# Kernel tuning notes

Measured on AMD Instinct MI355X. Metric: run time of the kernel, lower is better.

Reference implementation:

```python
import jax, jax.numpy as jnp
import numpy as np

DIM = 1536
NH = 12
HD = DIM // NH  # 128
FF, HH, WW = 32, 8, 12
L = FF * HH * WW  # 3072
WIN = (8, 4, 4)  # block of 128 tokens
BLK = WIN[0] * WIN[1] * WIN[2]


def rms_norm(x, g, eps=1e-5):
    # matches RMSNorm: normalize in fp32, scale by weight
    v = jnp.mean(jnp.square(x), axis=-1, keepdims=True)
    return x * jax.lax.rsqrt(v + eps) * g


def rope(x, freqs, n):
    # x: [B,S,D]; freqs: [S,1,HD/2,2] (cos,sin); complex rotation on pairs
    B, S, D = x.shape
    xr = x.reshape(B, S, n, D // n // 2, 2)
    c, s = freqs[..., 0], freqs[..., 1]        # [S,1,HD/2] broadcast over B,n
    a, b = xr[..., 0], xr[..., 1]
    out = jnp.stack([a * c - b * s, a * s + b * c], axis=-1)
    return out.reshape(B, S, D)


def partition3d(x, f, h, w):
    # [B,f,h,w,D] -> [B, nblocks, 128, D], block order (f/8, h/4, w/4)
    B, D = x.shape[0], x.shape[-1]
    wf, wh, ww = WIN
    x = x.reshape(B, f // wf, wf, h // wh, wh, w // ww, ww, D)
    x = x.transpose(0, 1, 3, 5, 2, 4, 6, 7)
    return x.reshape(B, -1, BLK, D)


def reverse3d(xw, f, h, w):
    # [B, nblocks, 128, D] -> [B, f*h*w, D]
    B, D = xw.shape[0], xw.shape[-1]
    wf, wh, ww = WIN
    x = xw.reshape(B, f // wf, h // wh, w // ww, wf, wh, ww, D)
    x = x.transpose(0, 1, 4, 2, 5, 3, 6, 7)
    return x.reshape(B, f * h * w, D)


def block_mask(f, h, w):
    # build_local_block_mask_3d: spatial mask is all-ones; temporal = context|local
    seqlen = f // WIN[0]
    nb_sp = (h // WIN[1]) * (w // WIN[2])
    stride = WIN[0]
    ctx_idx = (6 + stride - 1) // stride - 1          # context_frames=6
    radius = (5 + stride - 1) // stride               # temp_window_frames=5
    t = jnp.arange(seqlen)
    mt = (t[None, :] <= ctx_idx) | (jnp.abs(t[:, None] - t[None, :]) <= radius)
    # expand temporal block mask over spatial blocks -> [nb, nb]
    return jnp.repeat(jnp.repeat(mt, nb_sp, axis=0), nb_sp, axis=1)


def setup_inputs() -> dict:
    key = jax.random.key(0)
    ks = jax.random.split(key, 8)
    x = jax.random.normal(ks[0], (1, L, DIM), jnp.float32)
    ang = jax.random.uniform(ks[1], (L, 1, HD // 2), jnp.float32, 0.0, 2.0 * np.pi)
    freqs = jnp.stack([jnp.cos(ang), jnp.sin(ang)], axis=-1)  # [L,1,64,2]
    sc = 1.0 / np.sqrt(DIM)
    Wq = jax.random.normal(ks[2], (DIM, DIM), jnp.float32) * sc
    Wk = jax.random.normal(ks[3], (DIM, DIM), jnp.float32) * sc
    Wv = jax.random.normal(ks[4], (DIM, DIM), jnp.float32) * sc
    Wo = jax.random.normal(ks[5], (DIM, DIM), jnp.float32) * sc
    zeros = jnp.zeros((DIM,), jnp.float32)
    ones = jnp.ones((DIM,), jnp.float32)
    return {"x": x, "freqs": freqs, "Wq": Wq, "bq": zeros, "Wk": Wk, "bk": zeros,
            "Wv": Wv, "bv": zeros, "Wo": Wo, "bo": zeros, "g_q": ones, "g_k": ones,
            "f": FF, "h": HH, "w": WW, "local_range": 18}


def reference(x, freqs, Wq, bq, Wk, bk, Wv, bv, Wo, bo, g_q, g_k, f, h, w, local_range):
    B, S, D = x.shape
    q = rms_norm(x @ Wq + bq, g_q, eps=1e-5)
    k = rms_norm(x @ Wk + bk, g_k, eps=1e-5)
    v = x @ Wv + bv
    q = rope(q, freqs, NH)
    k = rope(k, freqs, NH)
    # window partition and flatten back to a reordered sequence
    qs = partition3d(q.reshape(B, f, h, w, D), f, h, w).reshape(B, S, D)
    ks_ = partition3d(k.reshape(B, f, h, w, D), f, h, w).reshape(B, S, D)
    vs = partition3d(v.reshape(B, f, h, w, D), f, h, w).reshape(B, S, D)
    bm = block_mask(f, h, w)                       # [nb, nb] bool
    tok_mask = jnp.repeat(jnp.repeat(bm, BLK, 0), BLK, 1)  # [S, S]
    qh = qs.reshape(B, S, NH, HD).transpose(0, 2, 1, 3)
    kh = ks_.reshape(B, S, NH, HD).transpose(0, 2, 1, 3)
    vh = vs.reshape(B, S, NH, HD).transpose(0, 2, 1, 3)
    scores = jnp.einsum('bhqd,bhkd->bhqk', qh, kh) / np.sqrt(HD)
    scores = jnp.where(tok_mask[None, None], scores, -jnp.inf)
    attn = jax.nn.softmax(scores, axis=-1)
    out = jnp.einsum('bhqk,bhkd->bhqd', attn, vh)
    out = out.transpose(0, 2, 1, 3).reshape(B, S, D)
    out = reverse3d(out.reshape(B, -1, BLK, D), f, h, w)  # undo window reorder
    return out @ Wo + bo
```

## Files before the change

### kernel.cpp

```cpp
#include <hip/hip_runtime.h>
#include <hip/hip_bf16.h>
#include <math.h>

#define S_LEN 3072
#define DMODEL 1536
#define NQKV 4608
#define NHEAD 12
#define HDIM 128
#define NSPLIT 3

typedef __attribute__((ext_vector_type(8))) short bf16x8;
typedef __attribute__((ext_vector_type(4))) float f32x4;

__device__ __forceinline__ void gload_lds16(const void* g, void* lds) {
  __builtin_amdgcn_global_load_lds(
      (const __attribute__((address_space(1))) unsigned int*)g,
      (__attribute__((address_space(3))) unsigned int*)lds, 16, 0, 0);
}

__device__ __forceinline__ int invperm(int p) {
  int blk = p >> 7;
  int w   = p & 127;
  int fb  = blk / 6;
  int rem = blk - fb * 6;
  int hb  = rem / 3;
  int wb  = rem - hb * 3;
  int fi  = fb * 8 + (w >> 4);
  int hi  = hb * 4 + ((w >> 2) & 3);
  int wi  = wb * 4 + (w & 3);
  return (fi * 8 + hi) * 12 + wi;
}

__device__ __forceinline__ int fwdperm(int s) {
  int fi = s / 96;
  int rem = s - fi * 96;
  int hi = rem / 12;
  int wi = rem - hi * 12;
  int fb = fi >> 3, wf = fi & 7;
  int hb = hi >> 2, wh = hi & 3;
  int wb = wi >> 2, ww = wi & 3;
  return ((fb * 2 + hb) * 3 + wb) * 128 + wf * 16 + wh * 4 + ww;
}

__device__ __forceinline__ void store_out(float* p, float v) { *p = v; }
__device__ __forceinline__ void store_out(__hip_bfloat16* p, float v) { *p = __float2bfloat16(v); }

__global__ __launch_bounds__(256) void convert_bias(
    const float* __restrict__ in, __hip_bfloat16* __restrict__ out,
    const float* __restrict__ bq, const float* __restrict__ bk,
    const float* __restrict__ bv, float* __restrict__ bqkv)
{
  if (blockIdx.x < 4608) {
    int i = blockIdx.x * 256 + threadIdx.x;
    float4 v = ((const float4*)in)[i];
    __hip_bfloat16 b[4] = {__float2bfloat16(v.x), __float2bfloat16(v.y),
                           __float2bfloat16(v.z), __float2bfloat16(v.w)};
    ((ushort4*)out)[i] = *(ushort4*)b;
  } else {
    int j = (blockIdx.x - 4608) * 256 + threadIdx.x;
    float v = (j < 1536) ? bq[j] : (j < 3072) ? bk[j - 1536] : bv[j - 3072];
    bqkv[j] = v;
  }
}

__global__ __launch_bounds__(256) void transpose_convert4(
    const float* __restrict__ W0, const float* __restrict__ W1,
    const float* __restrict__ W2, const float* __restrict__ W3,
    __hip_bfloat16* __restrict__ Wtqkv, __hip_bfloat16* __restrict__ Wot)
{
  __shared__ __hip_bfloat16 Ls[64][67];
  const int z = blockIdx.z;
  const float* W = (z == 0) ? W0 : (z == 1) ? W1 : (z == 2) ? W2 : W3;
  __hip_bfloat16* Wt = (z < 3) ? Wtqkv + (size_t)z * DMODEL * DMODEL : Wot;
  const int r0 = blockIdx.y * 64, c0 = blockIdx.x * 64, t = threadIdx.x;
  {
    int rr = t >> 2, cb = (t & 3) * 16;
    const float4* src = (const float4*)(W + (size_t)(r0 + rr) * DMODEL + c0 + cb);
    #pragma unroll
    for (int i = 0; i < 4; ++i) {
      float4 v = src[i];
      Ls[rr][cb + i * 4 + 0] = __float2bfloat16(v.x);
      Ls[rr][cb + i * 4 + 1] = __float2bfloat16(v.y);
      Ls[rr][cb + i * 4 + 2] = __float2bfloat16(v.z);
      Ls[rr][cb + i * 4 + 3] = __float2bfloat16(v.w);
    }
  }
  __syncthreads();
  {
    int cc = t >> 2, rb = (t & 3) * 16;
    unsigned short tmp[16];
    #pragma unroll
    for (int i = 0; i < 16; ++i) tmp[i] = *(unsigned short*)&Ls[rb + i][cc];
    uint4* dst = (uint4*)(Wt + (size_t)(c0 + cc) * DMODEL + r0 + rb);
    dst[0] = ((uint4*)tmp)[0];
    dst[1] = ((uint4*)tmp)[1];
  }
}

template <typename OutT, int BN>
__global__ __launch_bounds__(256) void gemm_bt(
    const __hip_bfloat16* __restrict__ A, const __hip_bfloat16* __restrict__ Bt,
    const float* __restrict__ bias, OutT* __restrict__ C, int M, int N, int K)
{
  constexpr int NB = BN / 32;
  __shared__ __hip_bfloat16 As[2][128 * 32];
  __shared__ __hip_bfloat16 Bs[2][BN * 32];
  const int tid = threadIdx.x, lane = tid & 63, wid = tid >> 6;
  const int l15 = lane & 15, l4 = lane >> 4;
  const int nwg = gridDim.x * gridDim.y;
  const int lin = blockIdx.y * gridDim.x + blockIdx.x;
  const int cpx = nwg >> 3;
  const int swz = (lin & 7) * cpx + (lin >> 3);
  const int row0 = (swz / gridDim.x) * 128, col0 = (swz % gridDim.x) * BN;
  const int wr = (wid >> 1) * 64, wc = (wid & 1) * (BN / 2);

  f32x4 acc[4][NB] = {};
  const char* Ab = (const char*)A;
  const char* Bb = (const char*)Bt;

  auto STAGE = [&](int buf, int k0) {
    #pragma unroll
    for (int i = 0; i < 2; ++i) {
      int slot = i * 256 + tid;
      int r = slot >> 2;
      int b = (slot & 3) * 16;
      gload_lds16(Ab + ((size_t)(row0 + r) * K + k0) * 2 + b,
                  (char*)As[buf] + ((size_t)i * 256 + wid * 64) * 16);
    }
    #pragma unroll
    for (int i = 0; i < BN / 64; ++i) {
      int slot = i * 256 + tid;
      int r = slot >> 2;
      int b = (slot & 3) * 16;
      gload_lds16(Bb + ((size_t)(col0 + r) * K + k0) * 2 + b,
                  (char*)Bs[buf] + ((size_t)i * 256 + wid * 64) * 16);
    }
  };

  STAGE(0, 0);
  __syncthreads();
  int cur = 0;
  for (int k0 = 0; k0 < K; k0 += 32) {
    if (k0 + 32 < K) STAGE(cur ^ 1, k0 + 32);
    bf16x8 a[4], b[NB];
    #pragma unroll
    for (int m = 0; m < 4; ++m)
      a[m] = *(const bf16x8*)&As[cur][(wr + m * 16 + l15) * 32 + l4 * 8];
    #pragma unroll
    for (int n = 0; n < NB; ++n)
      b[n] = *(const bf16x8*)&Bs[cur][(wc + n * 16 + l15) * 32 + l4 * 8];
    #pragma unroll
    for (int m = 0; m < 4; ++m)
      #pragma unroll
      for (int n = 0; n < NB; ++n)
        acc[m][n] = __builtin_amdgcn_mfma_f32_16x16x32_bf16(a[m], b[n], acc[m][n], 0, 0, 0);
    __syncthreads();
    cur ^= 1;
  }

  #pragma unroll
  for (int m = 0; m < 4; ++m) {
    #pragma unroll
    for (int r = 0; r < 4; ++r) {
      size_t row = row0 + wr + m * 16 + l4 * 4 + r;
      #pragma unroll
      for (int n = 0; n < NB; ++n) {
        int col = col0 + wc + n * 16 + l15;
        store_out(&C[row * N + col], acc[m][n][r] + bias[col]);
      }
    }
  }
}

__global__ __launch_bounds__(256) void norm_rope_perm(
    const __hip_bfloat16* __restrict__ X,
    const float* __restrict__ gq, const float* __restrict__ gk,
    const float* __restrict__ freqs,
    __hip_bfloat16* __restrict__ OutQ, __hip_bfloat16* __restrict__ OutK)
{
  const int s = blockIdx.x, tid = threadIdx.x;
  const int sec = blockIdx.y;
  const float* g = sec ? gk : gq;
  __hip_bfloat16* Out = sec ? OutK : OutQ;
  const float qsc = sec ? 1.0f : (0.08838834764831843f * 1.4426950408889634f);
  const unsigned int* row = (const unsigned int*)(X + (size_t)s * NQKV + sec * 1536);
  float e0[3], e1[3];
  float ss = 0.f;
  #pragma unroll
  for (int i = 0; i < 3; ++i) {
    unsigned int u = row[tid + i * 256];
    float a = __uint_as_float(u << 16);
    float b = __uint_as_float(u & 0xffff0000u);
    e0[i] = a; e1[i] = b;
    ss += a * a + b * b;
  }
  #pragma unroll
  for (int off = 32; off > 0; off >>= 1) ss += __shfl_down(ss, off, 64);
  __shared__ float wsum[4];
  if ((tid & 63) == 0) wsum[tid >> 6] = ss;
  __syncthreads();
  float rs = rsqrtf((wsum[0] + wsum[1] + wsum[2] + wsum[3]) * (1.f / DMODEL) + 1e-5f);
  rs *= qsc;
  const int p = fwdperm(s);
  #pragma unroll
  for (int i = 0; i < 3; ++i) {
    int pi = tid + i * 256;
    int n = pi >> 6, d2 = pi & 63;
    float c  = freqs[(size_t)s * 128 + 2 * d2];
    float sn = freqs[(size_t)s * 128 + 2 * d2 + 1];
    float y0 = e0[i] * rs * g[2 * pi];
    float y1 = e1[i] * rs * g[2 * pi + 1];
    float o0 = y0 * c - y1 * sn;
    float o1 = y0 * sn + y1 * c;
    __hip_bfloat16 b0 = __float2bfloat16(o0), b1 = __float2bfloat16(o1);
    unsigned int u = ((unsigned int)(*(unsigned short*)&b1) << 16) | (*(unsigned short*)&b0);
    ((unsigned int*)Out)[(((size_t)n * S_LEN + p) * HDIM + 2 * d2) >> 1] = u;
  }
}

__global__ __launch_bounds__(256) void v_transpose(
    const __hip_bfloat16* __restrict__ Vsec, __hip_bfloat16* __restrict__ Vt)
{
  __shared__ __hip_bfloat16 Ls[64][136];
  const int p0 = blockIdx.x * 64, h = blockIdx.y, t = threadIdx.x;
  {
    int pl = t & 63, dg = t >> 6;
    int sidx = invperm(p0 + pl);
    const uint4* src = (const uint4*)(Vsec + (size_t)sidx * NQKV + h * HDIM + dg * 32);
    #pragma unroll
    for (int i = 0; i < 4; ++i) {
      uint4 v = src[i];
      *(uint4*)&Ls[pl][dg * 32 + i * 8] = v;
    }
  }
  __syncthreads();
  {
    int d = t >> 1, ph = t & 1;
    unsigned short tmp[32];
    #pragma unroll
    for (int i = 0; i < 32; ++i) tmp[i] = *(unsigned short*)&Ls[ph * 32 + i][d];
    uint4* dst = (uint4*)(Vt + ((size_t)h * HDIM + d) * S_LEN + p0 + ph * 32);
    #pragma unroll
    for (int i = 0; i < 4; ++i) dst[i] = ((uint4*)tmp)[i];
  }
}

__global__ __launch_bounds__(512) void attn_mfma(
    const __hip_bfloat16* __restrict__ Qp, const __hip_bfloat16* __restrict__ Kp,
    const __hip_bfloat16* __restrict__ Vt,
    __hip_bfloat16* __restrict__ Opart, float* __restrict__ ml)
{
  __shared__ __hip_bfloat16 Ks[64 * 128];
  __shared__ __hip_bfloat16 Vs[128 * 64];
  __shared__ __align__(16) __hip_bfloat16 Pl[8][16][72];

  const int hw = blockIdx.x + 24 * (blockIdx.y + 3 * blockIdx.z);
  const int L  = (hw & 7) * 108 + (hw >> 3);
  const int j  = L % 6;
  const int t4 = (L / 6) & 3;
  const int sh = L / 24;
  const int h  = sh % 12;
  const int split = sh / 12;
  const int tg = (t4 == 0) ? 2 : (t4 == 1) ? 1 : (t4 == 2) ? 3 : 0;
  const int qb = tg * 6 + j;

  const int tid = threadIdx.x, lane = tid & 63, wid = tid >> 6;
  const int l15 = lane & 15, l4 = lane >> 4;

  const int NCh = (tg == 0) ? 8 : (tg == 2) ? 16 : 12;
  const int cbegin = split * NCh, cend = cbegin + NCh;

  const char* Kh = (const char*)(Kp + (size_t)h * S_LEN * HDIM);
  const char* Vh = (const char*)(Vt + (size_t)h * HDIM * S_LEN);

  unsigned int koffA, voffA;
  {
    unsigned int kr = tid >> 4;
    koffA = kr * 256 + (((tid & 15) * 16) ^ ((kr & 7) << 4));
    unsigned int vr = tid >> 3;
    voffA = vr * (S_LEN * 2) + (((tid & 7) * 16) ^ ((vr & 7) << 4));
  }

  auto k0_of = [&](int ci) { return ci * 64 + ((tg == 3 && ci >= 12) ? 768 : 0); };
  auto STAGE = [&](int k0) {
    const char* ks = Kh + (size_t)k0 * 256;
    gload_lds16(ks + koffA,        (char*)Ks + tid * 16);
    gload_lds16(ks + koffA + 8192, (char*)Ks + tid * 16 + 8192);
    const char* vs = Vh + (size_t)k0 * 2 + voffA;
    gload_lds16(vs,                          (char*)Vs + tid * 16);
    gload_lds16(vs + (size_t)64 * S_LEN * 2, (char*)Vs + tid * 16 + 8192);
  };

  bf16x8 aq[4];
  {
    const __hip_bfloat16* qr = Qp + (size_t)h * S_LEN * HDIM
        + (size_t)(qb * 128 + wid * 16 + l15) * HDIM + l4 * 8;
    #pragma unroll
    for (int dc = 0; dc < 4; ++dc) aq[dc] = *(const bf16x8*)(qr + dc * 32);
  }

  f32x4 oacc[8] = {};
  float m2v[4] = {-1e30f, -1e30f, -1e30f, -1e30f};
  float lsum[4] = {};

  for (int ci = cbegin; ci < cend; ++ci) {
    const int k0 = k0_of(ci);
    STAGE(k0);
    __syncthreads();

    f32x4 sfr[4] = {};
    #pragma unroll
    for (int ct = 0; ct < 4; ++ct) {
      int key = ct * 16 + l15;
      #pragma unroll
      for (int dc = 0; dc < 4; ++dc) {
        int b = (dc * 64 + l4 * 16) ^ ((l15 & 7) << 4);
        bf16x8 bk = *(const bf16x8*)((const char*)Ks + key * 256 + b);
        sfr[ct] = __builtin_amdgcn_mfma_f32_16x16x32_bf16(aq[dc], bk, sfr[ct], 0, 0, 0);
      }
    }
    float lmax[4];
    #pragma unroll
    for (int r = 0; r < 4; ++r)
      lmax[r] = fmaxf(fmaxf(sfr[0][r], sfr[1][r]), fmaxf(sfr[2][r], sfr[3][r]));
    bool grow = (lmax[0] > m2v[0] + 8.f) || (lmax[1] > m2v[1] + 8.f) ||
                (lmax[2] > m2v[2] + 8.f) || (lmax[3] > m2v[3] + 8.f);
    if (ci == cbegin || __any(grow)) {
      #pragma unroll
      for (int r = 0; r < 4; ++r) {
        float mx = lmax[r];
        #pragma unroll
        for (int o = 1; o < 16; o <<= 1) mx = fmaxf(mx, __shfl_xor(mx, o, 64));
        float mn = fmaxf(m2v[r], mx);
        float corr = exp2f(m2v[r] - mn);
        m2v[r] = mn;
        lsum[r] *= corr;
        #pragma unroll
        for (int n = 0; n < 8; ++n) oacc[n][r] *= corr;
      }
    }
    #pragma unroll
    for (int ct = 0; ct < 4; ++ct)
      #pragma unroll
      for (int r = 0; r < 4; ++r) {
        float p = exp2f(sfr[ct][r] - m2v[r]);
        lsum[r] += p;
        Pl[wid][l4 * 4 + r][ct * 16 + l15] = __float2bfloat16(p);
      }
    asm volatile("s_waitcnt lgkmcnt(0)" ::: "memory");
    __builtin_amdgcn_sched_barrier(0);
    #pragma unroll
    for (int ks = 0; ks < 2; ++ks) {
      bf16x8 pa = *(const bf16x8*)&Pl[wid][l15][ks * 32 + l4 * 8];
      #pragma unroll
      for (int n = 0; n < 8; ++n) {
        int d = n * 16 + l15;
        int b = (ks * 64 + l4 * 16) ^ ((d & 7) << 4);
        bf16x8 bv = *(const bf16x8*)((const char*)Vs + d * 128 + b);
        oacc[n] = __builtin_amdgcn_mfma_f32_16x16x32_bf16(pa, bv, oacc[n], 0, 0, 0);
      }
    }
    __syncthreads();
  }

  #pragma unroll
  for (int r = 0; r < 4; ++r) {
    float t = lsum[r];
    #pragma unroll
    for (int o = 1; o < 16; o <<= 1) t += __shfl_xor(t, o, 64);
    int qrow = qb * 128 + wid * 16 + l4 * 4 + r;
    size_t rowid = (size_t)(split * NHEAD + h) * S_LEN + qrow;
    float inv = 1.0f / t;
    __hip_bfloat16* dst = Opart + rowid * HDIM;
    #pragma unroll
    for (int n = 0; n < 8; ++n)
      dst[n * 16 + l15] = __float2bfloat16(oacc[n][r] * inv);
    if (l15 == 0) {
      ml[rowid * 2 + 0] = m2v[r];
      ml[rowid * 2 + 1] = t;
    }
  }
}

__global__ __launch_bounds__(256) void attn_merge(
    const __hip_bfloat16* __restrict__ Opart, const float* __restrict__ ml,
    __hip_bfloat16* __restrict__ AO)
{
  const int rid = blockIdx.x * 4 + (threadIdx.x >> 6);
  const int lane = threadIdx.x & 63;
  const int h = rid / S_LEN, q = rid - h * S_LEN;
  size_t rr[NSPLIT];
  float m[NSPLIT], l[NSPLIT];
  float mm = -1e30f;
  #pragma unroll
  for (int s = 0; s < NSPLIT; ++s) {
    rr[s] = (size_t)(s * NHEAD + h) * S_LEN + q;
    m[s] = ml[rr[s] * 2];
    l[s] = ml[rr[s] * 2 + 1];
    mm = fmaxf(mm, m[s]);
  }
  float wsum = 0.f, wgt[NSPLIT];
  #pragma unroll
  for (int s = 0; s < NSPLIT; ++s) { wgt[s] = l[s] * exp2f(m[s] - mm); wsum += wgt[s]; }
  float inv = 1.0f / wsum;
  float o0 = 0.f, o1 = 0.f;
  #pragma unroll
  for (int s = 0; s < NSPLIT; ++s) {
    unsigned int u = ((const unsigned int*)(Opart + rr[s] * HDIM))[lane];
    float a = wgt[s] * inv;
    o0 += a * __uint_as_float(u << 16);
    o1 += a * __uint_as_float(u & 0xffff0000u);
  }
  __hip_bfloat16 b0 = __float2bfloat16(o0), b1 = __float2bfloat16(o1);
  unsigned int u = ((unsigned int)(*(unsigned short*)&b1) << 16) | (*(unsigned short*)&b0);
  int sorig = invperm(q);
  ((unsigned int*)(AO + (size_t)sorig * DMODEL + h * HDIM))[lane] = u;
}

extern "C" void kernel_launch(void* const* d_in, const int* in_sizes, int n_in,
                              void* d_out, int out_size, void* d_ws, size_t ws_size,
                              hipStream_t stream)
{
  (void)in_sizes; (void)n_in; (void)out_size; (void)ws_size;
  const float* x     = (const float*)d_in[0];
  const float* freqs = (const float*)d_in[1];
  const float* Wq    = (const float*)d_in[2];
  const float* bq    = (const float*)d_in[3];
  const float* Wk    = (const float*)d_in[4];
  const float* bk    = (const float*)d_in[5];
  const float* Wv    = (const float*)d_in[6];
  const float* bv    = (const float*)d_in[7];
  const float* Wo    = (const float*)d_in[8];
  const float* bo    = (const float*)d_in[9];
  const float* gq    = (const float*)d_in[10];
  const float* gk    = (const float*)d_in[11];
  float* out = (float*)d_out;

  char* w = (char*)d_ws;
  __hip_bfloat16* xbf    = (__hip_bfloat16*)(w);
  __hip_bfloat16* Wtqkv  = (__hip_bfloat16*)(w + 9437184);
  __hip_bfloat16* Wot    = (__hip_bfloat16*)(w + 23592960);
  __hip_bfloat16* QKVbf  = (__hip_bfloat16*)(w + 28311552);
  __hip_bfloat16* Qp     = (__hip_bfloat16*)(w + 56623104);
  __hip_bfloat16* Kp     = (__hip_bfloat16*)(w + 66060288);
  __hip_bfloat16* Vtb    = (__hip_bfloat16*)(w + 75497472);
  __hip_bfloat16* AO     = (__hip_bfloat16*)(w + 84934656);
  float*          bqkv   = (float*)(w + 94371840);
  __hip_bfloat16* Opart  = QKVbf;
  float*          mlbuf  = (float*)(w);

  hipLaunchKernelGGL(convert_bias, dim3(4626), dim3(256), 0, stream,
                     x, xbf, bq, bk, bv, bqkv);
  hipLaunchKernelGGL(transpose_convert4, dim3(24, 24, 4), dim3(256), 0, stream,
                     Wq, Wk, Wv, Wo, Wtqkv, Wot);

  hipLaunchKernelGGL((gemm_bt<__hip_bfloat16, 128>), dim3(NQKV / 128, S_LEN / 128),
                     dim3(256), 0, stream, xbf, Wtqkv, bqkv, QKVbf, S_LEN, NQKV, DMODEL);

  hipLaunchKernelGGL(norm_rope_perm, dim3(S_LEN, 2), dim3(256), 0, stream,
                     QKVbf, gq, gk, freqs, Qp, Kp);
  hipLaunchKernelGGL(v_transpose, dim3(48, 12), dim3(256), 0, stream, QKVbf + 3072, Vtb);

  hipLaunchKernelGGL(attn_mfma, dim3(24, NSPLIT, NHEAD), dim3(512), 0, stream,
                     Qp, Kp, Vtb, Opart, mlbuf);
  hipLaunchKernelGGL(attn_merge, dim3(S_LEN * NHEAD / 4), dim3(256), 0, stream,
                     Opart, mlbuf, AO);

  hipLaunchKernelGGL((gemm_bt<float, 64>), dim3(DMODEL / 64, S_LEN / 128),
                     dim3(256), 0, stream, AO, Wot, bo, out, S_LEN, DMODEL, DMODEL);
}
```

Measured before the change: 241.6 us.

## Compute transposed S=K·Q^T so P stays in registers, dropping LDS round-trip

The QK^T MFMA now swaps its operands (K as A, Q as B), so each lane holds scores for one query column across several keys. Keys are assigned with a permuted index so the accumulator layout matches the A-operand layout of the PV MFMA. The probabilities can then be packed to bf16 directly in registers, with no write to and read from a shared-memory P buffer and no waitcnt barrier between them. Row max and sum reductions shrink to two cross-lane shuffles, at the cost of broadcasting correction and normalisation factors back to the output row layout with shuffles.

```diff
diff --git a/kernel.cpp b/kernel.cpp
--- a/kernel.cpp
+++ b/kernel.cpp
@@ -11,6 +11,7 @@
 
 typedef __attribute__((ext_vector_type(8))) short bf16x8;
 typedef __attribute__((ext_vector_type(4))) float f32x4;
+typedef __attribute__((ext_vector_type(4))) unsigned int u32x4;
 
 __device__ __forceinline__ void gload_lds16(const void* g, void* lds) {
   __builtin_amdgcn_global_load_lds(
@@ -252,7 +253,6 @@
 {
   __shared__ __hip_bfloat16 Ks[64 * 128];
   __shared__ __hip_bfloat16 Vs[128 * 64];
-  __shared__ __align__(16) __hip_bfloat16 Pl[8][16][72];
 
   const int hw = blockIdx.x + 24 * (blockIdx.y + 3 * blockIdx.z);
   const int L  = (hw & 7) * 108 + (hw >> 3);
@@ -273,6 +273,10 @@
   const char* Kh = (const char*)(Kp + (size_t)h * S_LEN * HDIM);
   const char* Vh = (const char*)(Vt + (size_t)h * HDIM * S_LEN);
 
+  const int kbase = 8 * (l15 >> 2) + (l15 & 3);
+  const int ksw0 = (l15 & 3) << 4;
+  const int ksw1 = (4 + (l15 & 3)) << 4;
+
   unsigned int koffA, voffA;
   {
     unsigned int kr = tid >> 4;
@@ -300,8 +304,8 @@
   }
 
   f32x4 oacc[8] = {};
-  float m2v[4] = {-1e30f, -1e30f, -1e30f, -1e30f};
-  float lsum[4] = {};
+  float m2 = -1e30f;
+  float lsum = 0.f;
 
   for (int ci = cbegin; ci < cend; ++ci) {
     const int k0 = k0_of(ci);
@@ -311,47 +315,63 @@
     f32x4 sfr[4] = {};
     #pragma unroll
     for (int ct = 0; ct < 4; ++ct) {
-      int key = ct * 16 + l15;
+      int key = kbase + (ct >> 1) * 32 + (ct & 1) * 4;
+      int swz = (ct & 1) ? ksw1 : ksw0;
       #pragma unroll
       for (int dc = 0; dc < 4; ++dc) {
-        int b = (dc * 64 + l4 * 16) ^ ((l15 & 7) << 4);
-        bf16x8 bk = *(const bf16x8*)((const char*)Ks + key * 256 + b);
-        sfr[ct] = __builtin_amdgcn_mfma_f32_16x16x32_bf16(aq[dc], bk, sfr[ct], 0, 0, 0);
+        int b = (dc * 64 + l4 * 16) ^ swz;
+        bf16x8 kf = *(const bf16x8*)((const char*)Ks + key * 256 + b);
+        sfr[ct] = __builtin_amdgcn_mfma_f32_16x16x32_bf16(kf, aq[dc], sfr[ct], 0, 0, 0);
       }
     }
-    float lmax[4];
-    #pragma unroll
-    for (int r = 0; r < 4; ++r)
-      lmax[r] = fmaxf(fmaxf(sfr[0][r], sfr[1][r]), fmaxf(sfr[2][r], sfr[3][r]));
-    bool grow = (lmax[0] > m2v[0] + 8.f) || (lmax[1] > m2v[1] + 8.f) ||
-                (lmax[2] > m2v[2] + 8.f) || (lmax[3] > m2v[3] + 8.f);
+    float lmax = fmaxf(
+        fmaxf(fmaxf(sfr[0][0], sfr[0][1]), fmaxf(sfr[0][2], sfr[0][3])),
+        fmaxf(fmaxf(fmaxf(sfr[1][0], sfr[1][1]), fmaxf(sfr[1][2], sfr[1][3])),
+              fmaxf(fmaxf(fmaxf(sfr[2][0], sfr[2][1]), fmaxf(sfr[2][2], sfr[2][3])),
+                    fmaxf(fmaxf(sfr[3][0], sfr[3][1]), fmaxf(sfr[3][2], sfr[3][3])))));
+    bool grow = lmax > m2 + 8.f;
     if (ci == cbegin || __any(grow)) {
+      float mf = lmax;
+      mf = fmaxf(mf, __shfl_xor(mf, 16, 64));
+      mf = fmaxf(mf, __shfl_xor(mf, 32, 64));
+      float mn = fmaxf(m2, mf);
+      float corr = exp2f(m2 - mn);
+      m2 = mn;
+      lsum *= corr;
+      float cr[4];
+      #pragma unroll
+      for (int r = 0; r < 4; ++r) cr[r] = __shfl(corr, l4 * 4 + r, 64);
+      #pragma unroll
+      for (int n = 0; n < 8; ++n)
+        #pragma unroll
+        for (int r = 0; r < 4; ++r) oacc[n][r] *= cr[r];
+    }
+    #pragma unroll
+    for (int ct = 0; ct < 4; ++ct)
       #pragma unroll
       for (int r = 0; r < 4; ++r) {
-        float mx = lmax[r];
-        #pragma unroll
-        for (int o = 1; o < 16; o <<= 1) mx = fmaxf(mx, __shfl_xor(mx, o, 64));
-        float mn = fmaxf(m2v[r], mx);
-        float corr = exp2f(m2v[r] - mn);
-        m2v[r] = mn;
-        lsum[r] *= corr;
-        #pragma unroll
-        for (int n = 0; n < 8; ++n) oacc[n][r] *= corr;
+        float p = exp2f(sfr[ct][r] - m2);
+        sfr[ct][r] = p;
+        lsum += p;
       }
-    }
-    #pragma unroll
-    for (int ct = 0; ct < 4; ++ct)
-      #pragma unroll
-      for (int r = 0; r < 4; ++r) {
-        float p = exp2f(sfr[ct][r] - m2v[r]);
-        lsum[r] += p;
-        Pl[wid][l4 * 4 + r][ct * 16 + l15] = __float2bfloat16(p);
+    #pragma unroll
+    for (int ks = 0; ks < 2; ++ks) {
+      u32x4 wv;
+      {
+        __hip_bfloat16 a0 = __float2bfloat16(sfr[2 * ks][0]);
+        __hip_bfloat16 a1 = __float2bfloat16(sfr[2 * ks][1]);
+        __hip_bfloat16 a2 = __float2bfloat16(sfr[2 * ks][2]);
+        __hip_bfloat16 a3 = __float2bfloat16(sfr[2 * ks][3]);
+        __hip_bfloat16 b0 = __float2bfloat16(sfr[2 * ks + 1][0]);
+        __hip_bfloat16 b1 = __float2bfloat16(sfr[2 * ks + 1][1]);
+        __hip_bfloat16 b2 = __float2bfloat16(sfr[2 * ks + 1][2]);
+        __hip_bfloat16 b3 = __float2bfloat16(sfr[2 * ks + 1][3]);
+        wv[0] = ((unsigned int)(*(unsigned short*)&a1) << 16) | (*(unsigned short*)&a0);
+        wv[1] = ((unsigned int)(*(unsigned short*)&a3) << 16) | (*(unsigned short*)&a2);
+        wv[2] = ((unsigned int)(*(unsigned short*)&b1) << 16) | (*(unsigned short*)&b0);
+        wv[3] = ((unsigned int)(*(unsigned short*)&b3) << 16) | (*(unsigned short*)&b2);
       }
-    asm volatile("s_waitcnt lgkmcnt(0)" ::: "memory");
-    __builtin_amdgcn_sched_barrier(0);
-    #pragma unroll
-    for (int ks = 0; ks < 2; ++ks) {
-      bf16x8 pa = *(const bf16x8*)&Pl[wid][l15][ks * 32 + l4 * 8];
+      bf16x8 pa = __builtin_bit_cast(bf16x8, wv);
       #pragma unroll
       for (int n = 0; n < 8; ++n) {
         int d = n * 16 + l15;
@@ -363,22 +383,25 @@
     __syncthreads();
   }
 
+  float t = lsum;
+  t += __shfl_xor(t, 16, 64);
+  t += __shfl_xor(t, 32, 64);
+  float inv = 1.0f / t;
   #pragma unroll
   for (int r = 0; r < 4; ++r) {
-    float t = lsum[r];
-    #pragma unroll
-    for (int o = 1; o < 16; o <<= 1) t += __shfl_xor(t, o, 64);
+    float invr = __shfl(inv, l4 * 4 + r, 64);
     int qrow = qb * 128 + wid * 16 + l4 * 4 + r;
     size_t rowid = (size_t)(split * NHEAD + h) * S_LEN + qrow;
-    float inv = 1.0f / t;
     __hip_bfloat16* dst = Opart + rowid * HDIM;
     #pragma unroll
     for (int n = 0; n < 8; ++n)
-      dst[n * 16 + l15] = __float2bfloat16(oacc[n][r] * inv);
-    if (l15 == 0) {
-      ml[rowid * 2 + 0] = m2v[r];
-      ml[rowid * 2 + 1] = t;
-    }
+      dst[n * 16 + l15] = __float2bfloat16(oacc[n][r] * invr);
+  }
+  if (lane < 16) {
+    int qrow = qb * 128 + wid * 16 + lane;
+    size_t rowid = (size_t)(split * NHEAD + h) * S_LEN + qrow;
+    ml[rowid * 2 + 0] = m2;
+    ml[rowid * 2 + 1] = t;
   }
 }
 
```

After: 253.6 us. 5.0% more time.
